# Kernel tuning notes

Measured on AMD Instinct MI355X. Metric: run time of the kernel, lower is better.

## Reference

```python
import jax, jax.numpy as jnp
import numpy as np


def setup_inputs() -> dict:
    key = jax.random.key(0)
    k1, k2 = jax.random.split(key)
    B, F, E, U = 16384, 39, 64, 128
    embeds = jax.random.normal(k1, (B, F, E), dtype=jnp.float32)
    outer_w = jax.random.normal(k2, (U, E, E), dtype=jnp.float32) * 0.05
    return {"embeds": embeds, "outer_w": outer_w}


def reference(embeds, outer_w):
    # embeds: (B, F, E) = concatenated field embeddings; outer_w: (U, E, E)
    feat_sum = jnp.sum(embeds, axis=1)  # (B, E)
    # lp[b,u] = sum_{i,j} feat_sum[b,i] * feat_sum[b,j] * outer_w[u,i,j]
    # == f^T W_u f, computed as a batched GEMM instead of the original's
    # per-unit elementwise multiply+reduce loop (same math).
    fw = jnp.einsum('bi,uij->buj', feat_sum, outer_w)  # (B, U, E)
    lp = jnp.einsum('buj,bj->bu', fw, feat_sum)        # (B, U)
    return lp
```

## Files before the change

### kernel.cpp

```cpp
#include <hip/hip_runtime.h>

#define B_TOTAL 16384
#define F 39
#define E 64
#define U 128
#define BT 64
#define THREADS 1024

typedef __attribute__((ext_vector_type(8))) short short8;
typedef __attribute__((ext_vector_type(4))) float f32x4;
typedef __attribute__((ext_vector_type(4))) unsigned u32x4;

__device__ __forceinline__ unsigned pack2_bf16(float a, float b) {
  unsigned ua = __builtin_bit_cast(unsigned, a) + 0x8000u;
  unsigned ub = __builtin_bit_cast(unsigned, b) + 0x8000u;
  return (ub & 0xFFFF0000u) | (ua >> 16);
}

__global__ __launch_bounds__(256) void prep_w(const float* __restrict__ w,
                                              u32x4* __restrict__ wf) {
  int tid = blockIdx.x * 256 + threadIdx.x;
  int lane = tid & 63;
  int frag = tid >> 6;
  int ks  = frag & 1;
  int ntg = (frag >> 1) & 7;
  int i   = frag >> 4;
  int uu  = ntg * 16 + (lane & 15);
  int k0  = ks * 32 + (lane >> 4) * 8;
  const f32x4* src = (const f32x4*)(w + (size_t)uu * (E * E) + i * E + k0);
  f32x4 v0 = __builtin_nontemporal_load(src);
  f32x4 v1 = __builtin_nontemporal_load(src + 1);
  u32x4 o;
  o[0] = pack2_bf16(v0[0], v0[1]);
  o[1] = pack2_bf16(v0[2], v0[3]);
  o[2] = pack2_bf16(v1[0], v1[1]);
  o[3] = pack2_bf16(v1[2], v1[3]);
  wf[tid] = o;
}

__global__ __launch_bounds__(THREADS) void fused_outer(
    const float* __restrict__ embeds, const u32x4* __restrict__ wf,
    float* __restrict__ out) {
  __shared__ __align__(16) char smem0[32768];
  __shared__ __align__(16) float FtT[E * 68];
  float* Ft  = (float*)smem0;
  f32x4* prt = (f32x4*)smem0;

  const int t = threadIdx.x;
  const int b0 = blockIdx.x * BT;

  {
    const int b = t >> 4, e4 = t & 15;
    const f32x4* src = (const f32x4*)(embeds + (size_t)(b0 + b) * (F * E)) + e4;
    f32x4 s = {0.f, 0.f, 0.f, 0.f};
    #pragma unroll
    for (int f = 0; f < F; ++f)
      s += __builtin_nontemporal_load(src + f * (E / 4));
    *(f32x4*)&Ft[b * 68 + e4 * 4] = s;
    FtT[(e4 * 4 + 0) * 68 + b] = s[0];
    FtT[(e4 * 4 + 1) * 68 + b] = s[1];
    FtT[(e4 * 4 + 2) * 68 + b] = s[2];
    FtT[(e4 * 4 + 3) * 68 + b] = s[3];
  }

  const int lane = t & 63, wave = t >> 6;
  const int uc = wave & 7;
  const int kh = wave >> 3;
  const int fl = lane & 15;
  const int fo = (lane >> 4) * 8;
  const int r0 = (lane >> 4) * 4;

  const u32x4* wv = wf + (size_t)(uc * 2) * 64 + lane;

  #define LOADW(buf, ii) {                 \
    buf[0] = wv[(size_t)((ii) * 16) * 64]; \
    buf[1] = wv[(size_t)((ii) * 16 + 1) * 64]; }

  const int i0 = kh * 32;
  u32x4 w0[2], w1[2], w2[2], w3[2];
  LOADW(w0, i0);
  LOADW(w1, i0 + 1);
  LOADW(w2, i0 + 2);
  LOADW(w3, i0 + 3);
  __syncthreads();

  short8 af[4][2];
  #pragma unroll
  for (int mt = 0; mt < 4; ++mt) {
    const float* fr = &Ft[(mt * 16 + fl) * 68];
    #pragma unroll
    for (int ks = 0; ks < 2; ++ks) {
      f32x4 v0 = *(const f32x4*)&fr[ks * 32 + fo];
      f32x4 v1 = *(const f32x4*)&fr[ks * 32 + fo + 4];
      u32x4 o;
      o[0] = pack2_bf16(v0[0], v0[1]);
      o[1] = pack2_bf16(v0[2], v0[3]);
      o[2] = pack2_bf16(v1[0], v1[1]);
      o[3] = pack2_bf16(v1[2], v1[3]);
      af[mt][ks] = __builtin_bit_cast(short8, o);
    }
  }
  __syncthreads();

  f32x4 acc[4];
  #pragma unroll
  for (int mt = 0; mt < 4; ++mt)
    #pragma unroll
    for (int r = 0; r < 4; ++r) acc[mt][r] = 0.f;

  #define STEP(ii, buf) {                                                      \
    short8 bf0 = __builtin_bit_cast(short8, buf[0]);                           \
    short8 bf1 = __builtin_bit_cast(short8, buf[1]);                           \
    _Pragma("unroll")                                                          \
    for (int mt = 0; mt < 4; ++mt) {                                           \
      f32x4 s = {0.f, 0.f, 0.f, 0.f};                                          \
      s = __builtin_amdgcn_mfma_f32_16x16x32_bf16(af[mt][0], bf0, s, 0, 0, 0); \
      s = __builtin_amdgcn_mfma_f32_16x16x32_bf16(af[mt][1], bf1, s, 0, 0, 0); \
      f32x4 fi = *(const f32x4*)&FtT[(ii) * 68 + mt * 16 + r0];                \
      acc[mt] += fi * s;                                                       \
    } }

  for (int i = i0; i < i0 + 32; i += 4) {
    STEP(i, w0);     LOADW(w0, i + 4);
    STEP(i + 1, w1); LOADW(w1, i + 5);
    STEP(i + 2, w2); LOADW(w2, i + 6);
    STEP(i + 3, w3); LOADW(w3, i + 7);
  }

  if (kh == 1) {
    #pragma unroll
    for (int mt = 0; mt < 4; ++mt)
      prt[(uc * 64 + lane) * 4 + mt] = acc[mt];
  }
  __syncthreads();
  if (kh == 0) {
    #pragma unroll
    for (int mt = 0; mt < 4; ++mt) {
      f32x4 v = acc[mt] + prt[(uc * 64 + lane) * 4 + mt];
      #pragma unroll
      for (int r = 0; r < 4; ++r)
        __builtin_nontemporal_store(
            v[r], &out[(size_t)(b0 + mt * 16 + r0 + r) * U + uc * 16 + fl]);
    }
  }
  #undef LOADW
  #undef STEP
}

extern "C" void kernel_launch(void* const* d_in, const int* in_sizes, int n_in,
                              void* d_out, int out_size, void* d_ws, size_t ws_size,
                              hipStream_t stream) {
  const float* embeds = (const float*)d_in[0];
  const float* w      = (const float*)d_in[1];
  float* out          = (float*)d_out;
  u32x4* wf           = (u32x4*)d_ws;
  prep_w<<<dim3(256), dim3(256), 0, stream>>>(w, wf);
  fused_outer<<<dim3(B_TOTAL / BT), dim3(THREADS), 0, stream>>>(embeds, wf, out);
}
```

Before: 231.7 us.

## Symmetrize outer weights to skip the lower-left quadratic-form block

prep_w now builds (W+W^T), halving the diagonal blocks and zeroing the lower-left 32x32 block of each unit's matrix. This uses the symmetry of f^T W f. The second K-half waves then run only one MFMA per i step instead of two, cutting total matrix work by a quarter. The cost is strided column reads in prep_w and an imbalance between the two wave groups, since the first group still does the full work per block.

```diff
diff --git a/kernel.cpp b/kernel.cpp
--- a/kernel.cpp
+++ b/kernel.cpp
@@ -27,14 +27,24 @@
   int i   = frag >> 4;
   int uu  = ntg * 16 + (lane & 15);
   int k0  = ks * 32 + (lane >> 4) * 8;
-  const f32x4* src = (const f32x4*)(w + (size_t)uu * (E * E) + i * E + k0);
-  f32x4 v0 = __builtin_nontemporal_load(src);
-  f32x4 v1 = __builtin_nontemporal_load(src + 1);
+  int ihi = i >> 5;
+  if (ihi && !ks) {
+    wf[tid] = (u32x4){0u, 0u, 0u, 0u};
+    return;
+  }
+  float c = (ihi == ks) ? 0.5f : 1.0f;
+  const float* rowp = w + (size_t)uu * (E * E) + i * E + k0;
+  const float* colp = w + (size_t)uu * (E * E) + (size_t)k0 * E + i;
+  f32x4 v0 = *(const f32x4*)rowp;
+  f32x4 v1 = *(const f32x4*)(rowp + 4);
+  float col[8];
+  #pragma unroll
+  for (int j = 0; j < 8; ++j) col[j] = colp[(size_t)j * E];
   u32x4 o;
-  o[0] = pack2_bf16(v0[0], v0[1]);
-  o[1] = pack2_bf16(v0[2], v0[3]);
-  o[2] = pack2_bf16(v1[0], v1[1]);
-  o[3] = pack2_bf16(v1[2], v1[3]);
+  o[0] = pack2_bf16(c * (v0[0] + col[0]), c * (v0[1] + col[1]));
+  o[1] = pack2_bf16(c * (v0[2] + col[2]), c * (v0[3] + col[3]));
+  o[2] = pack2_bf16(c * (v1[0] + col[4]), c * (v1[1] + col[5]));
+  o[3] = pack2_bf16(c * (v1[2] + col[6]), c * (v1[3] + col[7]));
   wf[tid] = o;
 }
 
@@ -70,18 +80,26 @@
   const int fo = (lane >> 4) * 8;
   const int r0 = (lane >> 4) * 4;
 
-  const u32x4* wv = wf + (size_t)(uc * 2) * 64 + lane;
+  const u32x4* wv  = wf + (size_t)(uc * 2) * 64 + lane;
+  const u32x4* wv1 = wf + (size_t)(uc * 2 + 1) * 64 + lane;
 
   #define LOADW(buf, ii) {                 \
     buf[0] = wv[(size_t)((ii) * 16) * 64]; \
     buf[1] = wv[(size_t)((ii) * 16 + 1) * 64]; }
+  #define LOADW1(dst, ii) { dst = wv1[(size_t)((ii) * 16) * 64]; }
 
-  const int i0 = kh * 32;
   u32x4 w0[2], w1[2], w2[2], w3[2];
-  LOADW(w0, i0);
-  LOADW(w1, i0 + 1);
-  LOADW(w2, i0 + 2);
-  LOADW(w3, i0 + 3);
+  if (kh == 0) {
+    LOADW(w0, 0);
+    LOADW(w1, 1);
+    LOADW(w2, 2);
+    LOADW(w3, 3);
+  } else {
+    LOADW1(w0[0], 32);
+    LOADW1(w1[0], 33);
+    LOADW1(w2[0], 34);
+    LOADW1(w3[0], 35);
+  }
   __syncthreads();
 
   short8 af[4][2];
@@ -120,11 +138,30 @@
       acc[mt] += fi * s;                                                       \
     } }
 
-  for (int i = i0; i < i0 + 32; i += 4) {
-    STEP(i, w0);     LOADW(w0, i + 4);
-    STEP(i + 1, w1); LOADW(w1, i + 5);
-    STEP(i + 2, w2); LOADW(w2, i + 6);
-    STEP(i + 3, w3); LOADW(w3, i + 7);
+  #define STEP1(ii, buf) {                                                     \
+    short8 bf1 = __builtin_bit_cast(short8, buf);                              \
+    _Pragma("unroll")                                                          \
+    for (int mt = 0; mt < 4; ++mt) {                                           \
+      f32x4 s = {0.f, 0.f, 0.f, 0.f};                                          \
+      s = __builtin_amdgcn_mfma_f32_16x16x32_bf16(af[mt][1], bf1, s, 0, 0, 0); \
+      f32x4 fi = *(const f32x4*)&FtT[(ii) * 68 + mt * 16 + r0];                \
+      acc[mt] += fi * s;                                                       \
+    } }
+
+  if (kh == 0) {
+    for (int i = 0; i < 32; i += 4) {
+      STEP(i, w0);     LOADW(w0, i + 4);
+      STEP(i + 1, w1); LOADW(w1, i + 5);
+      STEP(i + 2, w2); LOADW(w2, i + 6);
+      STEP(i + 3, w3); LOADW(w3, i + 7);
+    }
+  } else {
+    for (int i = 32; i < 64; i += 4) {
+      STEP1(i, w0[0]);     LOADW1(w0[0], i + 4);
+      STEP1(i + 1, w1[0]); LOADW1(w1[0], i + 5);
+      STEP1(i + 2, w2[0]); LOADW1(w2[0], i + 6);
+      STEP1(i + 3, w3[0]); LOADW1(w3[0], i + 7);
+    }
   }
 
   if (kh == 1) {
@@ -144,7 +181,9 @@
     }
   }
   #undef LOADW
+  #undef LOADW1
   #undef STEP
+  #undef STEP1
 }
 
 extern "C" void kernel_launch(void* const* d_in, const int* in_sizes, int n_in,
```

After: 231.1 us. No clear change (-0.3%).
